# Kernel optimization log

Measured on AMD Instinct MI355X. Metric: run time of the kernel, lower is better.

The kernel has to match this reference:

```python
import jax, jax.numpy as jnp
import numpy as np

N, E, R, H = 20000, 320000, 8, 4
KG, CC = 128, 4
IN, HID, OUT = 256, 256, 256  # in_channels = KG + 128 (GCN out)
HO1, HO2 = HID // H, OUT // H  # per-head out channels
SLOPE_ACT = 0.01   # nn.LeakyReLU default
SLOPE_ATT = 0.2    # RGATConv negative_slope default


def gcn_conv(x, W, b, src, dst):
    """PyG GCNConv: add self loops, symmetric norm, x@W, scatter-sum, +bias."""
    n = x.shape[0]
    loop = jnp.arange(n, dtype=src.dtype)
    s = jnp.concatenate([src, loop])
    d = jnp.concatenate([dst, loop])
    deg = jnp.zeros((n,), x.dtype).at[d].add(1.0)
    dis = jnp.where(deg > 0, jax.lax.rsqrt(jnp.maximum(deg, 1.0)), 0.0)
    norm = dis[s] * dis[d]                        # [E+N]
    h = x @ W                                     # [n, out]
    out = jax.ops.segment_sum(norm[:, None] * h[s], d, num_segments=n)
    return out + b


def rgat_conv(x, W, q, k, b, src, dst, edge_type, heads, oc):
    """PyG RGATConv (additive-self-attention, across-relation, dim=1, concat)."""
    n = x.shape[0]
    xw = jnp.einsum('ni,rio->rno', x, W)          # [R, n, heads*oc]
    out_i = xw[edge_type, dst]                    # [E, heads*oc]
    out_j = xw[edge_type, src]                    # [E, heads*oc]
    qi = out_i @ q                                # [E, heads]
    kj = out_j @ k                                # [E, heads]
    alpha = jax.nn.leaky_relu(qi + kj, SLOPE_ATT)
    # softmax over incoming edges per destination node (across-relation)
    amax = jax.ops.segment_max(alpha, dst, num_segments=n)[dst]
    ex = jnp.exp(alpha - amax)
    denom = jax.ops.segment_sum(ex, dst, num_segments=n)[dst]
    alpha = ex / denom                            # [E, heads]
    e = src.shape[0]
    msg = (alpha[:, :, None] * out_j.reshape(e, heads, oc)).reshape(e, heads * oc)
    out = jax.ops.segment_sum(msg, dst, num_segments=n) + b
    return out, alpha


def setup_inputs() -> dict:
    key = jax.random.key(0)
    ks = jax.random.split(key, 16)
    d = {}
    d['kg_emb'] = jax.random.normal(ks[0], (N, KG), jnp.float32)
    d['ccle0'] = jax.random.normal(ks[1], (N, CC), jnp.float32)
    d['gcn_w1'] = jax.random.normal(ks[2], (CC, 32), jnp.float32) / np.float32(np.sqrt(CC))
    d['gcn_b1'] = jnp.zeros((32,), jnp.float32)
    d['gcn_w2'] = jax.random.normal(ks[3], (32, 128), jnp.float32) / np.float32(np.sqrt(32))
    d['gcn_b2'] = jnp.zeros((128,), jnp.float32)
    d['rgat1_w'] = jax.random.normal(ks[4], (R, IN, HID), jnp.float32) / np.float32(np.sqrt(IN))
    d['rgat1_q'] = jax.random.normal(ks[5], (HID, H), jnp.float32) / np.float32(np.sqrt(HID))
    d['rgat1_k'] = jax.random.normal(ks[6], (HID, H), jnp.float32) / np.float32(np.sqrt(HID))
    d['rgat1_b'] = jnp.zeros((HID,), jnp.float32)
    d['rgat2_w'] = jax.random.normal(ks[7], (R, HID, OUT), jnp.float32) / np.float32(np.sqrt(HID))
    d['rgat2_q'] = jax.random.normal(ks[8], (OUT, H), jnp.float32) / np.float32(np.sqrt(OUT))
    d['rgat2_k'] = jax.random.normal(ks[9], (OUT, H), jnp.float32) / np.float32(np.sqrt(OUT))
    d['rgat2_b'] = jnp.zeros((OUT,), jnp.float32)
    d['lin_w'] = jax.random.normal(ks[10], (IN, OUT), jnp.float32) / np.float32(np.sqrt(IN))
    d['lin_b'] = jnp.zeros((OUT,), jnp.float32)
    d['edge_index'] = jax.random.randint(ks[11], (2, E), 0, N, jnp.int32)
    d['edge_type'] = jax.random.randint(ks[12], (E,), 0, R, jnp.int32)
    return d


def reference(kg_emb, ccle0, gcn_w1, gcn_b1, gcn_w2, gcn_b2,
              rgat1_w, rgat1_q, rgat1_k, rgat1_b,
              rgat2_w, rgat2_q, rgat2_k, rgat2_b,
              lin_w, lin_b, edge_index, edge_type):
    src, dst = edge_index[0], edge_index[1]
    # ccle_layer: GCN(4->32) -> LeakyReLU -> GCN(32->128)
    c = gcn_conv(ccle0, gcn_w1, gcn_b1, src, dst)
    c = jax.nn.leaky_relu(c, SLOPE_ACT)
    c = gcn_conv(c, gcn_w2, gcn_b2, src, dst)
    # node_id = arange(N): concat(kg_emb, ccle_out)
    x0 = jnp.concatenate([kg_emb, c], axis=1)     # [N, IN]
    h, a1 = rgat_conv(x0, rgat1_w, rgat1_q, rgat1_k, rgat1_b,
                      src, dst, edge_type, H, HO1)
    h = jax.nn.leaky_relu(h, SLOPE_ACT)           # dropout p=0 -> identity
    h, a2 = rgat_conv(h, rgat2_w, rgat2_q, rgat2_k, rgat2_b,
                      src, dst, edge_type, H, HO2)
    out = h + (x0 @ lin_w + lin_b)                # residual through self.lin
    return out, a1, a2
```

## Files before the change

### kernel.cpp

```cpp
#include <hip/hip_runtime.h>
#include <cstdint>

static constexpr int N = 20000;
static constexpr int E = 320000;
static constexpr int R = 8;
static constexpr int H = 4;
static constexpr int C = 256;

using short8 = __attribute__((ext_vector_type(8))) short;
using f32x4  = __attribute__((ext_vector_type(4))) float;
using us4    = __attribute__((ext_vector_type(4))) unsigned short;

__device__ __forceinline__ float lrelu(float x, float s) { return x >= 0.f ? x : s * x; }
__device__ __forceinline__ unsigned short f2bf(float f) {
    unsigned u = __float_as_uint(f);
    unsigned r = (u + 0x7FFFu + ((u >> 16) & 1u)) >> 16;
    return (unsigned short)r;
}
__device__ __forceinline__ float bf2f(unsigned short s) {
    return __uint_as_float(((unsigned)s) << 16);
}

__device__ __forceinline__ void gl2l16(const unsigned short* g, unsigned short* l) {
    __builtin_amdgcn_global_load_lds(
        (const __attribute__((address_space(1))) unsigned int*)g,
        (__attribute__((address_space(3))) unsigned int*)l, 16, 0, 0);
}

#define WTP 72

__device__ __forceinline__ void wconv_body(const float* __restrict__ W,
                                           unsigned short* __restrict__ Wt,
                                           int bid, unsigned short* T) {
    int z = bid >> 4;
    int tile = bid & 15;
    int k0 = (tile >> 2) * 64, n0 = (tile & 3) * 64;
    int t = threadIdx.x;
    const float* Wz = W + ((size_t)z << 16);
    int r = t >> 4;
    int cs = (t & 15) * 4;
#pragma unroll
    for (int rr = 0; rr < 4; ++rr) {
        int k = r + rr * 16;
        float4 v = *(const float4*)(Wz + (size_t)(k0 + k) * 256 + n0 + cs);
        T[(cs + 0) * WTP + k] = f2bf(v.x);
        T[(cs + 1) * WTP + k] = f2bf(v.y);
        T[(cs + 2) * WTP + k] = f2bf(v.z);
        T[(cs + 3) * WTP + k] = f2bf(v.w);
    }
    __syncthreads();
    int n = t >> 2, ck = (t & 3) * 16;
    unsigned short* dst = Wt + ((size_t)z << 16) + (size_t)(n0 + n) * 256 + k0 + ck;
    const unsigned short* srcp = T + n * WTP + ck;
    *(uint4*)(dst) = *(const uint4*)(srcp);
    *(uint4*)(dst + 8) = *(const uint4*)(srcp + 8);
}

__device__ __forceinline__ void wqkb_body(const float* __restrict__ W,
                                          const float* __restrict__ q,
                                          const float* __restrict__ kmat,
                                          unsigned short* __restrict__ wqkb,
                                          int w) {
    int lane = threadIdx.x & 63;
    int r = w >> 8, i = w & 255;
    const float* wr = W + ((size_t)(r * 256 + i)) * 256;
    float4 a = *(const float4*)(wr + lane * 4);
    float aq0 = 0.f, aq1 = 0.f, aq2 = 0.f, aq3 = 0.f;
    float ak0 = 0.f, ak1 = 0.f, ak2 = 0.f, ak3 = 0.f;
    int o = lane * 4;
    const float av[4] = {a.x, a.y, a.z, a.w};
#pragma unroll
    for (int j = 0; j < 4; ++j) {
        float4 qv = *(const float4*)(q + (o + j) * 4);
        float4 kv = *(const float4*)(kmat + (o + j) * 4);
        aq0 += av[j] * qv.x; aq1 += av[j] * qv.y;
        aq2 += av[j] * qv.z; aq3 += av[j] * qv.w;
        ak0 += av[j] * kv.x; ak1 += av[j] * kv.y;
        ak2 += av[j] * kv.z; ak3 += av[j] * kv.w;
    }
#pragma unroll
    for (int d = 1; d < 64; d <<= 1) {
        aq0 += __shfl_xor(aq0, d); aq1 += __shfl_xor(aq1, d);
        aq2 += __shfl_xor(aq2, d); aq3 += __shfl_xor(aq3, d);
        ak0 += __shfl_xor(ak0, d); ak1 += __shfl_xor(ak1, d);
        ak2 += __shfl_xor(ak2, d); ak3 += __shfl_xor(ak3, d);
    }
    if (lane == 0) {
        int nq = r * 4, nk = 32 + r * 4;
        wqkb[(nq + 0) * 256 + i] = f2bf(aq0);
        wqkb[(nq + 1) * 256 + i] = f2bf(aq1);
        wqkb[(nq + 2) * 256 + i] = f2bf(aq2);
        wqkb[(nq + 3) * 256 + i] = f2bf(aq3);
        wqkb[(nk + 0) * 256 + i] = f2bf(ak0);
        wqkb[(nk + 1) * 256 + i] = f2bf(ak1);
        wqkb[(nk + 2) * 256 + i] = f2bf(ak2);
        wqkb[(nk + 3) * 256 + i] = f2bf(ak3);
    }
}

__global__ __launch_bounds__(256) void k_prep(
    int* __restrict__ cnt,
    const float* __restrict__ cc0, const float* __restrict__ gw1,
    float* __restrict__ h1buf,
    const float* __restrict__ r1w, const float* __restrict__ r2w,
    const float* __restrict__ linw,
    unsigned short* __restrict__ wt, unsigned short* __restrict__ wt2,
    const float* __restrict__ r1q, const float* __restrict__ r1k,
    unsigned short* __restrict__ wqkb1,
    const float* __restrict__ r2q, const float* __restrict__ r2k,
    unsigned short* __restrict__ wqkb2)
{
    __shared__ unsigned short T[64 * WTP];
    int b = blockIdx.x;
    int t = threadIdx.x;
    if (b < 79) {
        int idx = b * 256 + t;
        if (idx < N) cnt[idx] = 0;
    } else if (b < 2579) {
        int idx = (b - 79) * 256 + t;
        if (idx < N * 32) {
            int n = idx >> 5, f = idx & 31;
            const float* xr = cc0 + n * 4;
            float acc = 0.f;
#pragma unroll
            for (int c = 0; c < 4; ++c) acc += xr[c] * gw1[c * 32 + f];
            h1buf[idx] = acc;
        }
    } else if (b < 2707) {
        wconv_body(r1w, wt, b - 2579, T);
    } else if (b < 2835) {
        wconv_body(r2w, wt2, b - 2707, T);
    } else if (b < 2851) {
        wconv_body(linw, wt + ((size_t)R << 16), b - 2835, T);
    } else if (b < 3363) {
        wqkb_body(r1w, r1q, r1k, wqkb1, ((b - 2851) * 256 + t) >> 6);
    } else {
        wqkb_body(r2w, r2q, r2k, wqkb2, ((b - 3363) * 256 + t) >> 6);
    }
}

__global__ void k_count(const int* __restrict__ ei, int* __restrict__ cnt) {
    int e = blockIdx.x * blockDim.x + threadIdx.x;
    if (e < E) atomicAdd(&cnt[ei[E + e]], 1);
}

__global__ __launch_bounds__(256) void k_scan_a(const int* __restrict__ cnt,
                                                int* __restrict__ loc,
                                                int* __restrict__ bsum) {
    __shared__ int sm[256];
    int t = threadIdx.x;
    int idx = blockIdx.x * 256 + t;
    int v = (idx < N) ? cnt[idx] : 0;
    sm[t] = v;
    __syncthreads();
#pragma unroll
    for (int off = 1; off < 256; off <<= 1) {
        int u = (t >= off) ? sm[t - off] : 0;
        __syncthreads();
        if (t >= off) sm[t] += u;
        __syncthreads();
    }
    if (idx < N) loc[idx] = sm[t] - v;
    if (t == 255) bsum[blockIdx.x] = sm[255];
}

__global__ __launch_bounds__(256) void k_scan_c(const int* __restrict__ cnt,
                                                const int* __restrict__ loc,
                                                const int* __restrict__ bsum,
                                                int* __restrict__ rowptr,
                                                int* __restrict__ cursor,
                                                float* __restrict__ dis) {
    __shared__ int wsum[4];
    __shared__ int smoff;
    int t = threadIdx.x;
    int part = 0;
    for (int j = t; j < blockIdx.x; j += 256) part += bsum[j];
#pragma unroll
    for (int d = 1; d < 64; d <<= 1) part += __shfl_xor(part, d);
    if ((t & 63) == 0) wsum[t >> 6] = part;
    __syncthreads();
    if (t == 0) smoff = wsum[0] + wsum[1] + wsum[2] + wsum[3];
    __syncthreads();
    int base = smoff;
    int idx = blockIdx.x * 256 + t;
    if (idx == 0) rowptr[N] = E;
    if (idx >= N) return;
    int run = base + loc[idx];
    rowptr[idx] = run;
    cursor[idx] = run;
    dis[idx] = rsqrtf((float)cnt[idx] + 1.0f);
}

__global__ void k_scatter(const int* __restrict__ ei, const int* __restrict__ et,
                          int* __restrict__ cursor, int* __restrict__ csr_se,
                          int* __restrict__ csr_eid) {
    int e = blockIdx.x * blockDim.x + threadIdx.x;
    if (e >= E) return;
    int d = ei[E + e];
    int pos = atomicAdd(&cursor[d], 1);
    csr_se[pos] = (et[e] << 16) | ei[e];
    csr_eid[pos] = e;
}

__global__ void k_agg32(const int* __restrict__ rowptr, const int* __restrict__ csr_se,
                        const float* __restrict__ dis, const float* __restrict__ h,
                        const float* __restrict__ b, float* __restrict__ c) {
    int idx = blockIdx.x * blockDim.x + threadIdx.x;
    if (idx >= N * 32) return;
    int d = idx >> 5, f = idx & 31;
    int beg = rowptr[d], end = rowptr[d + 1];
    float acc = 0.f;
    for (int i = beg; i < end; ++i) {
        int s = csr_se[i] & 0xFFFF;
        acc += dis[s] * h[s * 32 + f];
    }
    float dd = dis[d];
    c[idx] = dd * acc + dd * dd * h[idx] + b[f];
}

__global__ void k_h2kg(const float* __restrict__ c1, const float* __restrict__ W,
                       const float* __restrict__ kg, unsigned short* __restrict__ h,
                       float* __restrict__ x0, unsigned short* __restrict__ xb0) {
    int idx = blockIdx.x * blockDim.x + threadIdx.x;
    if (idx >= N * 128) return;
    int n = idx >> 7, f = idx & 127;
    const float* cr = c1 + n * 32;
    float acc = 0.f;
    for (int c = 0; c < 32; ++c) acc += lrelu(cr[c], 0.01f) * W[c * 128 + f];
    h[idx] = f2bf(acc);
    float v = kg[idx];
    x0[n * 256 + f] = v;
    xb0[n * 256 + f] = f2bf(v);
}

__global__ void k_agg128(const int* __restrict__ rowptr, const int* __restrict__ csr_se,
                         const float* __restrict__ dis,
                         const unsigned short* __restrict__ h,
                         const float* __restrict__ b, float* __restrict__ x0,
                         unsigned short* __restrict__ xb0) {
    int idx = blockIdx.x * blockDim.x + threadIdx.x;
    if (idx >= N * 128) return;
    int d = idx >> 7, f = idx & 127;
    int beg = rowptr[d], end = rowptr[d + 1];
    float acc = 0.f;
    int i = beg;
    for (; i + 2 <= end; i += 2) {
        int s0 = csr_se[i] & 0xFFFF;
        int s1 = csr_se[i + 1] & 0xFFFF;
        float d0 = dis[s0], d1 = dis[s1];
        float v0 = bf2f(h[s0 * 128 + f]), v1 = bf2f(h[s1 * 128 + f]);
        acc += d0 * v0 + d1 * v1;
    }
    if (i < end) {
        int s = csr_se[i] & 0xFFFF;
        acc += dis[s] * bf2f(h[s * 128 + f]);
    }
    float dd = dis[d];
    float v = dd * acc + dd * dd * bf2f(h[d * 128 + f]) + b[f];
    x0[d * 256 + 128 + f] = v;
    xb0[d * 256 + 128 + f] = f2bf(v);
}

#define QP 264
__global__ __launch_bounds__(256) void k_qnkn_mfma(
    const unsigned short* __restrict__ xb, const unsigned short* __restrict__ wqkb,
    float* __restrict__ qn, float* __restrict__ kn)
{
    __shared__ unsigned short Ws[64 * QP];
    int t = threadIdx.x;
    {
        int r = t >> 2, off = (t & 3) * 64;
#pragma unroll
        for (int i = 0; i < 8; ++i)
            *(uint4*)(&Ws[r * QP + off + i * 8]) =
                *(const uint4*)(wqkb + r * 256 + off + i * 8);
    }
    __syncthreads();
    int wave = t >> 6, lane = t & 63;
    int lrow = lane & 15, kq = lane >> 4;
    int mw = blockIdx.x * 64 + wave * 16;
    int gm = mw + lrow;
    int gmc = gm < N ? gm : N - 1;

    f32x4 acc[4];
#pragma unroll
    for (int j = 0; j < 4; ++j) acc[j] = (f32x4){0.f, 0.f, 0.f, 0.f};

    for (int k0 = 0; k0 < 8; ++k0) {
        short8 af = *(const short8*)(xb + (size_t)gmc * 256 + k0 * 32 + kq * 8);
#pragma unroll
        for (int j = 0; j < 4; ++j) {
            short8 bf4 = *(const short8*)(&Ws[(j * 16 + lrow) * QP + k0 * 32 + kq * 8]);
            acc[j] = __builtin_amdgcn_mfma_f32_16x16x32_bf16(bf4, af, acc[j], 0, 0, 0);
        }
    }
    if (gm < N) {
#pragma unroll
        for (int j = 0; j < 4; ++j) {
            int colb = j * 16 + kq * 4;
            float4 v = {acc[j][0], acc[j][1], acc[j][2], acc[j][3]};
            if (colb < 32) *(float4*)(qn + (size_t)gm * 32 + colb) = v;
            else           *(float4*)(kn + (size_t)gm * 32 + (colb - 32)) = v;
        }
    }
}

__global__ void k_soft(const int* __restrict__ rowptr, const int* __restrict__ csr_se,
                       const int* __restrict__ csr_eid,
                       const float* __restrict__ qn, const float* __restrict__ kn,
                       float* __restrict__ alpha_csr, float* __restrict__ aout) {
    int wid = (blockIdx.x * blockDim.x + threadIdx.x) >> 6;
    int lane = threadIdx.x & 63;
    if (wid >= N) return;
    int d = wid;
    int beg = rowptr[d], end = rowptr[d + 1];
    if (beg >= end) return;
    int slot = lane >> 2, h = lane & 3;
    int nc = (end - beg + 15) >> 4;
    const float* qrow = qn + d * 32;

    auto rawv = [&](int i) {
        int se = csr_se[i];
        int tt = se >> 16, s = se & 0xFFFF;
        return lrelu(qrow[tt * 4 + h] + kn[s * 32 + tt * 4 + h], 0.2f);
    };

    float av[4];
    float m = -1e30f;
    for (int c = 0; c < nc; ++c) {
        int i = beg + c * 16 + slot;
        float v = (i < end) ? rawv(i) : -1e30f;
        if (c < 4) av[c] = v;
        m = fmaxf(m, v);
    }
    m = fmaxf(m, __shfl_xor(m, 4));
    m = fmaxf(m, __shfl_xor(m, 8));
    m = fmaxf(m, __shfl_xor(m, 16));
    m = fmaxf(m, __shfl_xor(m, 32));

    float sum = 0.f;
    for (int c = 0; c < nc; ++c) {
        int i = beg + c * 16 + slot;
        float ex = 0.f;
        if (i < end) {
            float v = (c < 4) ? av[c] : rawv(i);
            ex = expf(v - m);
        }
        if (c < 4) av[c] = ex;
        sum += ex;
    }
    sum += __shfl_xor(sum, 4);
    sum += __shfl_xor(sum, 8);
    sum += __shfl_xor(sum, 16);
    sum += __shfl_xor(sum, 32);
    float inv = 1.f / sum;

    for (int c = 0; c < nc; ++c) {
        int i = beg + c * 16 + slot;
        if (i < end) {
            float ex = (c < 4) ? av[c] : expf(rawv(i) - m);
            float a = ex * inv;
            alpha_csr[i * 4 + h] = a;
            aout[csr_eid[i] * 4 + h] = a;
        }
    }
}

__global__ __launch_bounds__(256) void k_soft_gather(
    const int* __restrict__ rowptr, const int* __restrict__ csr_se,
    const int* __restrict__ csr_eid,
    const float* __restrict__ qn, const float* __restrict__ kn,
    const unsigned short* __restrict__ xw,
    const float* __restrict__ bias, float* __restrict__ out,
    unsigned short* __restrict__ xbout, float* __restrict__ aout,
    int first, int act)
{
    int node = blockIdx.x * 4 + (threadIdx.x >> 6);
    if (node >= N) return;
    int lane = threadIdx.x & 63;
    int slot = lane >> 2, h = lane & 3;
    int hsel = lane >> 4;
    int beg = rowptr[node], end = rowptr[node + 1];
    float ax = 0.f, ay = 0.f, az = 0.f, aw = 0.f;
    const unsigned short* xwl = xw + lane * 4;

    if (beg < end) {
        int nc = (end - beg + 15) >> 4;
        const float* qrow = qn + node * 32;
        auto rawv_se = [&](int se) {
            int tt = se >> 16, s = se & 0xFFFF;
            return lrelu(qrow[tt * 4 + h] + kn[s * 32 + tt * 4 + h], 0.2f);
        };

        float av[4]; int sev[4];
        float m = -1e30f;
        for (int c = 0; c < nc; ++c) {
            int i = beg + c * 16 + slot;
            float v = -1e30f; int se = 0;
            if (i < end) { se = csr_se[i]; v = rawv_se(se); }
            if (c < 4) { av[c] = v; sev[c] = se; }
            m = fmaxf(m, v);
        }
        m = fmaxf(m, __shfl_xor(m, 4));
        m = fmaxf(m, __shfl_xor(m, 8));
        m = fmaxf(m, __shfl_xor(m, 16));
        m = fmaxf(m, __shfl_xor(m, 32));

        float sum = 0.f;
        for (int c = 0; c < nc; ++c) {
            int i = beg + c * 16 + slot;
            float ex = 0.f;
            if (i < end) {
                float v = (c < 4) ? av[c] : rawv_se(csr_se[i]);
                ex = expf(v - m);
            }
            if (c < 4) av[c] = ex;
            sum += ex;
        }
        sum += __shfl_xor(sum, 4);
        sum += __shfl_xor(sum, 8);
        sum += __shfl_xor(sum, 16);
        sum += __shfl_xor(sum, 32);
        float inv = 1.f / sum;

        for (int c = 0; c < nc; ++c) {
            int i = beg + c * 16 + slot;
            float a = 0.f;
            int se = 0;
            if (i < end) {
                float ex;
                if (c < 4) { ex = av[c]; se = sev[c]; }
                else       { se = csr_se[i]; ex = expf(rawv_se(se) - m); }
                a = ex * inv;
                aout[csr_eid[i] * 4 + h] = a;
            }
            int ne = end - (beg + c * 16);
            if (ne > 16) ne = 16;
            for (int e = 0; e < ne; e += 4) {
                int rr = ne - e;
                int e1 = (rr > 1) ? e + 1 : e;
                int e2 = (rr > 2) ? e + 2 : e;
                int e3 = (rr > 3) ? e + 3 : e;
                float ag0 = __shfl(a, (e  << 2) | hsel);
                float ag1 = __shfl(a, (e1 << 2) | hsel); if (rr <= 1) ag1 = 0.f;
                float ag2 = __shfl(a, (e2 << 2) | hsel); if (rr <= 2) ag2 = 0.f;
                float ag3 = __shfl(a, (e3 << 2) | hsel); if (rr <= 3) ag3 = 0.f;
                int sg0 = __shfl(se, e  << 2);
                int sg1 = __shfl(se, e1 << 2);
                int sg2 = __shfl(se, e2 << 2);
                int sg3 = __shfl(se, e3 << 2);
                uint2 v0 = *(const uint2*)(xwl + ((size_t)(sg0 >> 16) * N + (sg0 & 0xFFFF)) * 256);
                uint2 v1 = *(const uint2*)(xwl + ((size_t)(sg1 >> 16) * N + (sg1 & 0xFFFF)) * 256);
                uint2 v2 = *(const uint2*)(xwl + ((size_t)(sg2 >> 16) * N + (sg2 & 0xFFFF)) * 256);
                uint2 v3 = *(const uint2*)(xwl + ((size_t)(sg3 >> 16) * N + (sg3 & 0xFFFF)) * 256);
                ax += ag0 * __uint_as_float(v0.x << 16);
                ay += ag0 * __uint_as_float(v0.x & 0xFFFF0000u);
                az += ag0 * __uint_as_float(v0.y << 16);
                aw += ag0 * __uint_as_float(v0.y & 0xFFFF0000u);
                ax += ag1 * __uint_as_float(v1.x << 16);
                ay += ag1 * __uint_as_float(v1.x & 0xFFFF0000u);
                az += ag1 * __uint_as_float(v1.y << 16);
                aw += ag1 * __uint_as_float(v1.y & 0xFFFF0000u);
                ax += ag2 * __uint_as_float(v2.x << 16);
                ay += ag2 * __uint_as_float(v2.x & 0xFFFF0000u);
                az += ag2 * __uint_as_float(v2.y << 16);
                aw += ag2 * __uint_as_float(v2.y & 0xFFFF0000u);
                ax += ag3 * __uint_as_float(v3.x << 16);
                ay += ag3 * __uint_as_float(v3.x & 0xFFFF0000u);
                az += ag3 * __uint_as_float(v3.y << 16);
                aw += ag3 * __uint_as_float(v3.y & 0xFFFF0000u);
            }
        }
    }

    float* o = out + (size_t)node * 256 + lane * 4;
    float vx, vy, vz, vw;
    if (first) {
        float4 b = *(const float4*)(bias + lane * 4);
        vx = ax + b.x; vy = ay + b.y; vz = az + b.z; vw = aw + b.w;
    } else {
        float4 q = *(const float4*)o;
        vx = q.x + ax; vy = q.y + ay; vz = q.z + az; vw = q.w + aw;
    }
    if (act) {
        vx = lrelu(vx, 0.01f); vy = lrelu(vy, 0.01f);
        vz = lrelu(vz, 0.01f); vw = lrelu(vw, 0.01f);
        us4 xv = {f2bf(vx), f2bf(vy), f2bf(vz), f2bf(vw)};
        *(us4*)(xbout + (size_t)node * 256 + lane * 4) = xv;
    }
    float4 v = {vx, vy, vz, vw};
    *(float4*)o = v;
}

#define TM 128
#define TN 128
__global__ __launch_bounds__(256) void gemm_mfma4(
    const unsigned short* __restrict__ A, const unsigned short* __restrict__ Bt,
    unsigned short* __restrict__ Cbf, float* __restrict__ Cf,
    const float* __restrict__ bias, const float* __restrict__ bias2,
    int M, int NZ, int NT, int MT, int zlin)
{
    __shared__ unsigned short As[128 * 32];
    __shared__ unsigned short Bs[128 * 32];

    int bi = blockIdx.x;
    int cx = bi & 7;
    int g = bi >> 3;
    int per = NZ * NT;
    int mh = g / per;
    int j  = g % per;
    int mt = mh * 8 + cx;
    if (mt >= MT) return;
    int z  = j % NZ;
    int nb = j / NZ;
    int m0 = mt * TM;
    int n0 = nb * TN;

    const unsigned short* Bz = Bt + ((size_t)z << 16);
    int t = threadIdx.x;
    int wave = t >> 6, lane = t & 63;
    int wr = wave >> 1, wc = wave & 1;
    int lrow = lane & 15, kq = lane >> 4;

    int sr0 = (wave * 2 + 0) * 16 + (lane >> 2);
    int sr1 = (wave * 2 + 1) * 16 + (lane >> 2);
    int sc = (((lane & 3) ^ ((lane >> 3) & 3))) * 8;
    int gm0 = m0 + sr0; if (gm0 >= M) gm0 = M - 1;
    int gm1 = m0 + sr1; if (gm1 >= M) gm1 = M - 1;
    const unsigned short* gA0 = A + (size_t)gm0 * 256 + sc;
    const unsigned short* gA1 = A + (size_t)gm1 * 256 + sc;
    const unsigned short* gB0 = Bz + (size_t)(n0 + sr0) * 256 + sc;
    const unsigned short* gB1 = Bz + (size_t)(n0 + sr1) * 256 + sc;
    unsigned short* lA0 = &As[(wave * 2 + 0) * 512];
    unsigned short* lA1 = &As[(wave * 2 + 1) * 512];
    unsigned short* lB0 = &Bs[(wave * 2 + 0) * 512];
    unsigned short* lB1 = &Bs[(wave * 2 + 1) * 512];

    int rg = (kq ^ ((lrow >> 1) & 3)) * 8;

    f32x4 acc[4][4];
#pragma unroll
    for (int i = 0; i < 4; ++i)
#pragma unroll
        for (int jj = 0; jj < 4; ++jj) acc[i][jj] = (f32x4){0.f, 0.f, 0.f, 0.f};

    for (int k0 = 0; k0 < 256; k0 += 32) {
        gl2l16(gA0 + k0, lA0);
        gl2l16(gA1 + k0, lA1);
        gl2l16(gB0 + k0, lB0);
        gl2l16(gB1 + k0, lB1);
        __syncthreads();
        short8 af[4], bf4[4];
#pragma unroll
        for (int i = 0; i < 4; ++i)
            af[i] = *(const short8*)(&As[(wr * 64 + i * 16 + lrow) * 32 + rg]);
#pragma unroll
        for (int jj = 0; jj < 4; ++jj)
            bf4[jj] = *(const short8*)(&Bs[(wc * 64 + jj * 16 + lrow) * 32 + rg]);
#pragma unroll
        for (int i = 0; i < 4; ++i)
#pragma unroll
            for (int jj = 0; jj < 4; ++jj)
                acc[i][jj] = __builtin_amdgcn_mfma_f32_16x16x32_bf16(bf4[jj], af[i],
                                                                     acc[i][jj], 0, 0, 0);
        __syncthreads();
    }
    if (z == zlin) {
#pragma unroll
        for (int i = 0; i < 4; ++i) {
            int gm = m0 + wr * 64 + i * 16 + lrow;
            if (gm >= M) continue;
#pragma unroll
            for (int jj = 0; jj < 4; ++jj) {
                int gnb = n0 + wc * 64 + jj * 16 + kq * 4;
                float4 b1 = *(const float4*)(bias + gnb);
                float4 b2 = *(const float4*)(bias2 + gnb);
                float4 v = {acc[i][jj][0] + b1.x + b2.x,
                            acc[i][jj][1] + b1.y + b2.y,
                            acc[i][jj][2] + b1.z + b2.z,
                            acc[i][jj][3] + b1.w + b2.w};
                *(float4*)(Cf + (size_t)gm * 256 + gnb) = v;
            }
        }
    } else {
#pragma unroll
        for (int i = 0; i < 4; ++i) {
            int gm = m0 + wr * 64 + i * 16 + lrow;
            if (gm >= M) continue;
#pragma unroll
            for (int jj = 0; jj < 4; ++jj) {
                int gnb = n0 + wc * 64 + jj * 16 + kq * 4;
                us4 v = {f2bf(acc[i][jj][0]), f2bf(acc[i][jj][1]),
                         f2bf(acc[i][jj][2]), f2bf(acc[i][jj][3])};
                *(us4*)(Cbf + ((size_t)z * M + gm) * 256 + gnb) = v;
            }
        }
    }
}

__global__ __launch_bounds__(256) void k_msg_gather(
    const int* __restrict__ rowptr, const int* __restrict__ csr_se,
    const float* __restrict__ alpha_csr, const unsigned short* __restrict__ xw,
    const float* __restrict__ bias, float* __restrict__ out,
    unsigned short* __restrict__ xbout, int r0, int r1, int first, int act) {
    int node = blockIdx.x * 4 + (threadIdx.x >> 6);
    if (node >= N) return;
    int lane = threadIdx.x & 63;
    int hsel = lane >> 4;
    int beg = rowptr[node], end = rowptr[node + 1];
    float ax = 0.f, ay = 0.f, az = 0.f, aw = 0.f;
    const unsigned short* xwl = xw + lane * 4;

    for (int i = beg; i < end; ++i) {
        int se = csr_se[i];
        int tt = se >> 16;
        if (tt >= r0 && tt < r1) {
            int s = se & 0xFFFF;
            float a = alpha_csr[i * 4 + hsel];
            uint2 pv = *(const uint2*)(xwl + ((size_t)(tt - r0) * N + s) * 256);
            ax += a * __uint_as_float(pv.x << 16);
            ay += a * __uint_as_float(pv.x & 0xFFFF0000u);
            az += a * __uint_as_float(pv.y << 16);
            aw += a * __uint_as_float(pv.y & 0xFFFF0000u);
        }
    }

    float* o = out + (size_t)node * 256 + lane * 4;
    float vx, vy, vz, vw;
    if (first) {
        float4 b = *(const float4*)(bias + lane * 4);
        vx = ax + b.x; vy = ay + b.y; vz = az + b.z; vw = aw + b.w;
    } else {
        float4 q = *(const float4*)o;
        vx = q.x + ax; vy = q.y + ay; vz = q.z + az; vw = q.w + aw;
    }
    if (act) {
        vx = lrelu(vx, 0.01f); vy = lrelu(vy, 0.01f);
        vz = lrelu(vz, 0.01f); vw = lrelu(vw, 0.01f);
        us4 xv = {f2bf(vx), f2bf(vy), f2bf(vz), f2bf(vw)};
        *(us4*)(xbout + (size_t)node * 256 + lane * 4) = xv;
    }
    float4 v = {vx, vy, vz, vw};
    *(float4*)o = v;
}

extern "C" void kernel_launch(void* const* d_in, const int* in_sizes, int n_in,
                              void* d_out, int out_size, void* d_ws, size_t ws_size,
                              hipStream_t stream) {
    const float* kg   = (const float*)d_in[0];
    const float* cc0  = (const float*)d_in[1];
    const float* gw1  = (const float*)d_in[2];
    const float* gb1  = (const float*)d_in[3];
    const float* gw2  = (const float*)d_in[4];
    const float* gb2  = (const float*)d_in[5];
    const float* r1w  = (const float*)d_in[6];
    const float* r1q  = (const float*)d_in[7];
    const float* r1k  = (const float*)d_in[8];
    const float* r1b  = (const float*)d_in[9];
    const float* r2w  = (const float*)d_in[10];
    const float* r2q  = (const float*)d_in[11];
    const float* r2k  = (const float*)d_in[12];
    const float* r2b  = (const float*)d_in[13];
    const float* linw = (const float*)d_in[14];
    const float* linb = (const float*)d_in[15];
    const int*   ei   = (const int*)d_in[16];
    const int*   et   = (const int*)d_in[17];

    float* out = (float*)d_out;
    float* a1  = out + (size_t)N * C;
    float* a2  = a1 + (size_t)E * H;

    float* ws = (float*)d_ws;
    size_t off = 0;
    float* dis  = ws + off; off += N;
    float* h1   = ws + off; off += (size_t)N * 32;
    float* c1   = ws + off; off += (size_t)N * 32;
    unsigned short* h2b = (unsigned short*)(ws + off); off += (size_t)N * 64;
    float* x0   = ws + off; off += (size_t)N * C;
    float* hmid = ws + off; off += (size_t)N * C;
    float* qn   = ws + off; off += (size_t)N * R * H;
    float* kn   = ws + off; off += (size_t)N * R * H;
    int* cnt     = (int*)(ws + off); off += N;
    int* rowptr  = (int*)(ws + off); off += N + 1;
    int* cursor  = (int*)(ws + off); off += N;
    int* scanloc = (int*)(ws + off); off += N;
    int* scanbs  = (int*)(ws + off); off += 256;
    int* csr_se  = (int*)(ws + off); off += E;
    int* csr_eid = (int*)(ws + off); off += E;
    float* alpha = ws + off; off += (size_t)E * H;
    unsigned short* xb0 = (unsigned short*)(ws + off); off += (size_t)N * 128;
    unsigned short* xb1 = (unsigned short*)(ws + off); off += (size_t)N * 128;
    unsigned short* wt  = (unsigned short*)(ws + off); off += (size_t)(R + 1) * 32768;
    unsigned short* wt2 = (unsigned short*)(ws + off); off += (size_t)R * 32768;
    unsigned short* wtl = wt + ((size_t)R << 16);
    unsigned short* wqkb1 = (unsigned short*)(ws + off); off += 8192;
    unsigned short* wqkb2 = (unsigned short*)(ws + off); off += 8192;
    unsigned short* xwb = (unsigned short*)(ws + off);

    size_t fixedB = off * 4;
    int K = R;
    if (ws_size > fixedB) {
        size_t kmax = (ws_size - fixedB) / ((size_t)N * C * 2);
        if (kmax < (size_t)K) K = (int)kmax;
    } else {
        K = 1;
    }
    if (K < 1) K = 1;

    const int B = 256;
    auto cdiv = [](long a, long b) { return (int)((a + b - 1) / b); };
    const int MT = cdiv(N, TM);
    const int NT = C / TN;
    const int NB = cdiv(N, 256);

    k_prep<<<3875, 256, 0, stream>>>(cnt, cc0, gw1, h1,
                                     r1w, r2w, linw, wt, wt2,
                                     r1q, r1k, wqkb1, r2q, r2k, wqkb2);

    k_count<<<cdiv(E, B), B, 0, stream>>>(ei, cnt);
    k_scan_a<<<NB, 256, 0, stream>>>(cnt, scanloc, scanbs);
    k_scan_c<<<NB, 256, 0, stream>>>(cnt, scanloc, scanbs, rowptr, cursor, dis);
    k_scatter<<<cdiv(E, B), B, 0, stream>>>(ei, et, cursor, csr_se, csr_eid);

    k_agg32<<<cdiv((long)N * 32, B), B, 0, stream>>>(rowptr, csr_se, dis, h1, gb1, c1);
    k_h2kg<<<cdiv((long)N * 128, B), B, 0, stream>>>(c1, gw2, kg, h2b, x0, xb0);
    k_agg128<<<cdiv((long)N * 128, B), B, 0, stream>>>(rowptr, csr_se, dis, h2b,
                                                       gb2, x0, xb0);

    auto rgat = [&](unsigned short* xb, const unsigned short* wqkb_l,
                    const unsigned short* wt_l, const float* b,
                    float* obuf, unsigned short* xbout, float* aout,
                    int first, int act, int lin, float* linout,
                    const float* lb1, const float* lb2) {
        k_qnkn_mfma<<<cdiv(N, 64), B, 0, stream>>>(xb, wqkb_l, qn, kn);
        if (K == R) {
            int nz = R + (lin ? 1 : 0);
            int zl = lin ? R : -1;
            int gx = 8 * nz * NT * cdiv(MT, 8);
            gemm_mfma4<<<gx, 256, 0, stream>>>(xb, wt_l, xwb, linout, lb1, lb2,
                                               N, nz, NT, MT, zl);
            k_soft_gather<<<cdiv(N, 4), B, 0, stream>>>(
                rowptr, csr_se, csr_eid, qn, kn, xwb, b, obuf, xbout, aout,
                first, act);
        } else {
            k_soft<<<cdiv((long)N * 64, B), B, 0, stream>>>(rowptr, csr_se, csr_eid,
                                                            qn, kn, alpha, aout);
            for (int r0 = 0; r0 < R; r0 += K) {
                int kc = (R - r0) < K ? (R - r0) : K;
                int addlin = (lin && (r0 + kc == R)) ? 1 : 0;
                int nz = kc + addlin;
                int zl = addlin ? kc : -1;
                int gx = 8 * nz * NT * cdiv(MT, 8);
                gemm_mfma4<<<gx, 256, 0, stream>>>(xb, wt_l + ((size_t)r0 << 16), xwb,
                                                   linout, lb1, lb2,
                                                   N, nz, NT, MT, zl);
                int last = (r0 + kc >= R) ? 1 : 0;
                k_msg_gather<<<cdiv(N, 4), 256, 0, stream>>>(
                    rowptr, csr_se, alpha, xwb, b, obuf, xbout, r0, r0 + kc,
                    (first && r0 == 0) ? 1 : 0, act && last);
            }
        }
    };

    rgat(xb0, wqkb1, wt, r1b, hmid, xb1, a1, 1, 1,
         1, out, linb, r2b);

    rgat(xb1, wqkb2, wt2, r2b, out, nullptr, a2, 0, 0,
         0, nullptr, nullptr, nullptr);
}
```

Before: 436.1 us.

## Fold q/k projection into relation GEMM launch and interleave CSR src/eid arrays

The separate q/k projection kernel is removed in the fast path. It becomes an extra tile column of the relation GEMM, with the q/k weight buffer padded to 128 rows of zeros so the existing 128-wide tile loader works unchanged. The CSR source/type and edge-id arrays are merged into one int2 array, so the softmax-gather kernel gets both with a single load. This saves one launch per layer and one scattered load per edge. In exchange it wastes half of each q/k tile on zero rows, and aggregation kernels that only need .x now fetch twice the bytes.

```diff
diff --git a/kernel.cpp b/kernel.cpp
--- a/kernel.cpp
+++ b/kernel.cpp
@@ -134,8 +134,16 @@
         wconv_body(linw, wt + ((size_t)R << 16), b - 2835, T);
     } else if (b < 3363) {
         wqkb_body(r1w, r1q, r1k, wqkb1, ((b - 2851) * 256 + t) >> 6);
+    } else if (b < 3875) {
+        wqkb_body(r2w, r2q, r2k, wqkb2, ((b - 3363) * 256 + t) >> 6);
+    } else if (b < 3883) {
+        int idx = (b - 3875) * 256 + t;
+        uint4 z4 = {0, 0, 0, 0};
+        *(uint4*)(wqkb1 + 64 * 256 + idx * 8) = z4;
     } else {
-        wqkb_body(r2w, r2q, r2k, wqkb2, ((b - 3363) * 256 + t) >> 6);
+        int idx = (b - 3883) * 256 + t;
+        uint4 z4 = {0, 0, 0, 0};
+        *(uint4*)(wqkb2 + 64 * 256 + idx * 8) = z4;
     }
 }
 
@@ -192,17 +200,16 @@
 }
 
 __global__ void k_scatter(const int* __restrict__ ei, const int* __restrict__ et,
-                          int* __restrict__ cursor, int* __restrict__ csr_se,
-                          int* __restrict__ csr_eid) {
+                          int* __restrict__ cursor, int2* __restrict__ csr) {
     int e = blockIdx.x * blockDim.x + threadIdx.x;
     if (e >= E) return;
     int d = ei[E + e];
     int pos = atomicAdd(&cursor[d], 1);
-    csr_se[pos] = (et[e] << 16) | ei[e];
-    csr_eid[pos] = e;
-}
-
-__global__ void k_agg32(const int* __restrict__ rowptr, const int* __restrict__ csr_se,
+    int2 v = { (et[e] << 16) | ei[e], e };
+    csr[pos] = v;
+}
+
+__global__ void k_agg32(const int* __restrict__ rowptr, const int2* __restrict__ csr,
                         const float* __restrict__ dis, const float* __restrict__ h,
                         const float* __restrict__ b, float* __restrict__ c) {
     int idx = blockIdx.x * blockDim.x + threadIdx.x;
@@ -211,7 +218,7 @@
     int beg = rowptr[d], end = rowptr[d + 1];
     float acc = 0.f;
     for (int i = beg; i < end; ++i) {
-        int s = csr_se[i] & 0xFFFF;
+        int s = csr[i].x & 0xFFFF;
         acc += dis[s] * h[s * 32 + f];
     }
     float dd = dis[d];
@@ -233,7 +240,7 @@
     xb0[n * 256 + f] = f2bf(v);
 }
 
-__global__ void k_agg128(const int* __restrict__ rowptr, const int* __restrict__ csr_se,
+__global__ void k_agg128(const int* __restrict__ rowptr, const int2* __restrict__ csr,
                          const float* __restrict__ dis,
                          const unsigned short* __restrict__ h,
                          const float* __restrict__ b, float* __restrict__ x0,
@@ -245,14 +252,14 @@
     float acc = 0.f;
     int i = beg;
     for (; i + 2 <= end; i += 2) {
-        int s0 = csr_se[i] & 0xFFFF;
-        int s1 = csr_se[i + 1] & 0xFFFF;
+        int s0 = csr[i].x & 0xFFFF;
+        int s1 = csr[i + 1].x & 0xFFFF;
         float d0 = dis[s0], d1 = dis[s1];
         float v0 = bf2f(h[s0 * 128 + f]), v1 = bf2f(h[s1 * 128 + f]);
         acc += d0 * v0 + d1 * v1;
     }
     if (i < end) {
-        int s = csr_se[i] & 0xFFFF;
+        int s = csr[i].x & 0xFFFF;
         acc += dis[s] * bf2f(h[s * 128 + f]);
     }
     float dd = dis[d];
@@ -305,8 +312,7 @@
     }
 }
 
-__global__ void k_soft(const int* __restrict__ rowptr, const int* __restrict__ csr_se,
-                       const int* __restrict__ csr_eid,
+__global__ void k_soft(const int* __restrict__ rowptr, const int2* __restrict__ csr,
                        const float* __restrict__ qn, const float* __restrict__ kn,
                        float* __restrict__ alpha_csr, float* __restrict__ aout) {
     int wid = (blockIdx.x * blockDim.x + threadIdx.x) >> 6;
@@ -320,7 +326,7 @@
     const float* qrow = qn + d * 32;
 
     auto rawv = [&](int i) {
-        int se = csr_se[i];
+        int se = csr[i].x;
         int tt = se >> 16, s = se & 0xFFFF;
         return lrelu(qrow[tt * 4 + h] + kn[s * 32 + tt * 4 + h], 0.2f);
     };
@@ -361,14 +367,13 @@
             float ex = (c < 4) ? av[c] : expf(rawv(i) - m);
             float a = ex * inv;
             alpha_csr[i * 4 + h] = a;
-            aout[csr_eid[i] * 4 + h] = a;
+            aout[csr[i].y * 4 + h] = a;
         }
     }
 }
 
 __global__ __launch_bounds__(256) void k_soft_gather(
-    const int* __restrict__ rowptr, const int* __restrict__ csr_se,
-    const int* __restrict__ csr_eid,
+    const int* __restrict__ rowptr, const int2* __restrict__ csr,
     const float* __restrict__ qn, const float* __restrict__ kn,
     const unsigned short* __restrict__ xw,
     const float* __restrict__ bias, float* __restrict__ out,
@@ -392,13 +397,13 @@
             return lrelu(qrow[tt * 4 + h] + kn[s * 32 + tt * 4 + h], 0.2f);
         };
 
-        float av[4]; int sev[4];
+        float av[4]; int2 sev[4];
         float m = -1e30f;
         for (int c = 0; c < nc; ++c) {
             int i = beg + c * 16 + slot;
-            float v = -1e30f; int se = 0;
-            if (i < end) { se = csr_se[i]; v = rawv_se(se); }
-            if (c < 4) { av[c] = v; sev[c] = se; }
+            float v = -1e30f; int2 ce = {0, 0};
+            if (i < end) { ce = csr[i]; v = rawv_se(ce.x); }
+            if (c < 4) { av[c] = v; sev[c] = ce; }
             m = fmaxf(m, v);
         }
         m = fmaxf(m, __shfl_xor(m, 4));
@@ -411,7 +416,7 @@
             int i = beg + c * 16 + slot;
             float ex = 0.f;
             if (i < end) {
-                float v = (c < 4) ? av[c] : rawv_se(csr_se[i]);
+                float v = (c < 4) ? av[c] : rawv_se(csr[i].x);
                 ex = expf(v - m);
             }
             if (c < 4) av[c] = ex;
@@ -428,11 +433,12 @@
             float a = 0.f;
             int se = 0;
             if (i < end) {
-                float ex;
-                if (c < 4) { ex = av[c]; se = sev[c]; }
-                else       { se = csr_se[i]; ex = expf(rawv_se(se) - m); }
+                float ex; int2 ce;
+                if (c < 4) { ex = av[c]; ce = sev[c]; }
+                else       { ce = csr[i]; ex = expf(rawv_se(ce.x) - m); }
                 a = ex * inv;
-                aout[csr_eid[i] * 4 + h] = a;
+                se = ce.x;
+                aout[ce.y * 4 + h] = a;
             }
             int ne = end - (beg + c * 16);
             if (ne > 16) ne = 16;
@@ -498,7 +504,9 @@
     const unsigned short* __restrict__ A, const unsigned short* __restrict__ Bt,
     unsigned short* __restrict__ Cbf, float* __restrict__ Cf,
     const float* __restrict__ bias, const float* __restrict__ bias2,
-    int M, int NZ, int NT, int MT, int zlin)
+    const unsigned short* __restrict__ Bqk,
+    float* __restrict__ qn, float* __restrict__ kn,
+    int M, int NZ, int NT, int MT, int zlin, int qks)
 {
     __shared__ unsigned short As[128 * 32];
     __shared__ unsigned short Bs[128 * 32];
@@ -506,17 +514,18 @@
     int bi = blockIdx.x;
     int cx = bi & 7;
     int g = bi >> 3;
-    int per = NZ * NT;
+    int per = NZ * NT + (qks >= 0 ? 1 : 0);
     int mh = g / per;
     int j  = g % per;
     int mt = mh * 8 + cx;
     if (mt >= MT) return;
-    int z  = j % NZ;
-    int nb = j / NZ;
+    bool isqk = (qks >= 0 && j == NZ * NT);
+    int z = 0, nb = 0;
+    if (!isqk) { z = j % NZ; nb = j / NZ; }
     int m0 = mt * TM;
     int n0 = nb * TN;
 
-    const unsigned short* Bz = Bt + ((size_t)z << 16);
+    const unsigned short* Bz = isqk ? Bqk : (Bt + ((size_t)z << 16));
     int t = threadIdx.x;
     int wave = t >> 6, lane = t & 63;
     int wr = wave >> 1, wc = wave & 1;
@@ -565,7 +574,23 @@
                                                                      acc[i][jj], 0, 0, 0);
         __syncthreads();
     }
-    if (z == zlin) {
+    if (isqk) {
+        if (wc == 0) {
+#pragma unroll
+            for (int i = 0; i < 4; ++i) {
+                int gm = m0 + wr * 64 + i * 16 + lrow;
+                if (gm >= M) continue;
+#pragma unroll
+                for (int jj = 0; jj < 4; ++jj) {
+                    int gnb = jj * 16 + kq * 4;
+                    float4 v = {acc[i][jj][0], acc[i][jj][1],
+                                acc[i][jj][2], acc[i][jj][3]};
+                    if (gnb < 32) *(float4*)(qn + (size_t)gm * 32 + gnb) = v;
+                    else          *(float4*)(kn + (size_t)gm * 32 + (gnb - 32)) = v;
+                }
+            }
+        }
+    } else if (z == zlin) {
 #pragma unroll
         for (int i = 0; i < 4; ++i) {
             int gm = m0 + wr * 64 + i * 16 + lrow;
@@ -599,7 +624,7 @@
 }
 
 __global__ __launch_bounds__(256) void k_msg_gather(
-    const int* __restrict__ rowptr, const int* __restrict__ csr_se,
+    const int* __restrict__ rowptr, const int2* __restrict__ csr,
     const float* __restrict__ alpha_csr, const unsigned short* __restrict__ xw,
     const float* __restrict__ bias, float* __restrict__ out,
     unsigned short* __restrict__ xbout, int r0, int r1, int first, int act) {
@@ -612,7 +637,7 @@
     const unsigned short* xwl = xw + lane * 4;
 
     for (int i = beg; i < end; ++i) {
-        int se = csr_se[i];
+        int se = csr[i].x;
         int tt = se >> 16;
         if (tt >= r0 && tt < r1) {
             int s = se & 0xFFFF;
@@ -685,16 +710,14 @@
     int* cursor  = (int*)(ws + off); off += N;
     int* scanloc = (int*)(ws + off); off += N;
     int* scanbs  = (int*)(ws + off); off += 256;
-    int* csr_se  = (int*)(ws + off); off += E;
-    int* csr_eid = (int*)(ws + off); off += E;
+    int2* csr    = (int2*)(ws + off); off += (size_t)E * 2;
     float* alpha = ws + off; off += (size_t)E * H;
     unsigned short* xb0 = (unsigned short*)(ws + off); off += (size_t)N * 128;
     unsigned short* xb1 = (unsigned short*)(ws + off); off += (size_t)N * 128;
     unsigned short* wt  = (unsigned short*)(ws + off); off += (size_t)(R + 1) * 32768;
     unsigned short* wt2 = (unsigned short*)(ws + off); off += (size_t)R * 32768;
-    unsigned short* wtl = wt + ((size_t)R << 16);
-    unsigned short* wqkb1 = (unsigned short*)(ws + off); off += 8192;
-    unsigned short* wqkb2 = (unsigned short*)(ws + off); off += 8192;
+    unsigned short* wqkb1 = (unsigned short*)(ws + off); off += 16384;
+    unsigned short* wqkb2 = (unsigned short*)(ws + off); off += 16384;
     unsigned short* xwb = (unsigned short*)(ws + off);
 
     size_t fixedB = off * 4;
@@ -713,18 +736,18 @@
     const int NT = C / TN;
     const int NB = cdiv(N, 256);
 
-    k_prep<<<3875, 256, 0, stream>>>(cnt, cc0, gw1, h1,
+    k_prep<<<3891, 256, 0, stream>>>(cnt, cc0, gw1, h1,
                                      r1w, r2w, linw, wt, wt2,
                                      r1q, r1k, wqkb1, r2q, r2k, wqkb2);
 
     k_count<<<cdiv(E, B), B, 0, stream>>>(ei, cnt);
     k_scan_a<<<NB, 256, 0, stream>>>(cnt, scanloc, scanbs);
     k_scan_c<<<NB, 256, 0, stream>>>(cnt, scanloc, scanbs, rowptr, cursor, dis);
-    k_scatter<<<cdiv(E, B), B, 0, stream>>>(ei, et, cursor, csr_se, csr_eid);
-
-    k_agg32<<<cdiv((long)N * 32, B), B, 0, stream>>>(rowptr, csr_se, dis, h1, gb1, c1);
+    k_scatter<<<cdiv(E, B), B, 0, stream>>>(ei, et, cursor, csr);
+
+    k_agg32<<<cdiv((long)N * 32, B), B, 0, stream>>>(rowptr, csr, dis, h1, gb1, c1);
     k_h2kg<<<cdiv((long)N * 128, B), B, 0, stream>>>(c1, gw2, kg, h2b, x0, xb0);
-    k_agg128<<<cdiv((long)N * 128, B), B, 0, stream>>>(rowptr, csr_se, dis, h2b,
+    k_agg128<<<cdiv((long)N * 128, B), B, 0, stream>>>(rowptr, csr, dis, h2b,
                                                        gb2, x0, xb0);
 
     auto rgat = [&](unsigned short* xb, const unsigned short* wqkb_l,
@@ -732,18 +755,19 @@
                     float* obuf, unsigned short* xbout, float* aout,
                     int first, int act, int lin, float* linout,
                     const float* lb1, const float* lb2) {
-        k_qnkn_mfma<<<cdiv(N, 64), B, 0, stream>>>(xb, wqkb_l, qn, kn);
         if (K == R) {
             int nz = R + (lin ? 1 : 0);
             int zl = lin ? R : -1;
-            int gx = 8 * nz * NT * cdiv(MT, 8);
+            int per = nz * NT + 1;
+            int gx = 8 * per * cdiv(MT, 8);
             gemm_mfma4<<<gx, 256, 0, stream>>>(xb, wt_l, xwb, linout, lb1, lb2,
-                                               N, nz, NT, MT, zl);
+                                               wqkb_l, qn, kn,
+                                               N, nz, NT, MT, zl, nz * NT);
             k_soft_gather<<<cdiv(N, 4), B, 0, stream>>>(
-                rowptr, csr_se, csr_eid, qn, kn, xwb, b, obuf, xbout, aout,
-                first, act);
+                rowptr, csr, qn, kn, xwb, b, obuf, xbout, aout, first, act);
         } else {
-            k_soft<<<cdiv((long)N * 64, B), B, 0, stream>>>(rowptr, csr_se, csr_eid,
+            k_qnkn_mfma<<<cdiv(N, 64), B, 0, stream>>>(xb, wqkb_l, qn, kn);
+            k_soft<<<cdiv((long)N * 64, B), B, 0, stream>>>(rowptr, csr,
                                                             qn, kn, alpha, aout);
             for (int r0 = 0; r0 < R; r0 += K) {
                 int kc = (R - r0) < K ? (R - r0) : K;
@@ -753,10 +777,11 @@
                 int gx = 8 * nz * NT * cdiv(MT, 8);
                 gemm_mfma4<<<gx, 256, 0, stream>>>(xb, wt_l + ((size_t)r0 << 16), xwb,
                                                    linout, lb1, lb2,
-                                                   N, nz, NT, MT, zl);
+                                                   nullptr, nullptr, nullptr,
+                                                   N, nz, NT, MT, zl, -1);
                 int last = (r0 + kc >= R) ? 1 : 0;
                 k_msg_gather<<<cdiv(N, 4), 256, 0, stream>>>(
-                    rowptr, csr_se, alpha, xwb, b, obuf, xbout, r0, r0 + kc,
+                    rowptr, csr, alpha, xwb, b, obuf, xbout, r0, r0 + kc,
                     (first && r0 == 0) ? 1 : 0, act && last);
             }
         }
```

After: 466.8 us. 7.0% more time.
